# Kernel tuning notes

Measured on AMD Instinct MI355X. Metric: run time of the kernel, lower is better.

## Reference

```python
import jax, jax.numpy as jnp
import numpy as np

EPS = 1e-5  # torch LayerNorm default


def setup_inputs() -> dict:
    key = jax.random.key(0)
    ks = jax.random.split(key, 7)
    B, s, i, c, h = 1, 1024, 512, 8, 8
    scale = 0.1
    return {
        "m": jax.random.normal(ks[0], (B, s, i, c), dtype=jnp.float32),
        "ln_gamma": jnp.ones((c,), dtype=jnp.float32),
        "ln_beta": jnp.zeros((c,), dtype=jnp.float32),
        "Wq": jax.random.normal(ks[1], (c * h, c), dtype=jnp.float32) * scale,
        "Wk": jax.random.normal(ks[2], (c, c), dtype=jnp.float32) * scale,
        "Wv": jax.random.normal(ks[3], (c, c), dtype=jnp.float32) * scale,
        "Wg": jax.random.normal(ks[4], (c * h, c), dtype=jnp.float32) * scale,
        "Wo": jax.random.normal(ks[5], (c, c * h), dtype=jnp.float32) * scale,
        "bo": jnp.zeros((c,), dtype=jnp.float32),
    }


def reference(m, ln_gamma, ln_beta, Wq, Wk, Wv, Wg, Wo, bo):
    c = Wk.shape[0]
    h = Wq.shape[0] // c
    B, s, i, _ = m.shape

    # LayerNorm over the channel dim c
    mu = jnp.mean(m, axis=-1, keepdims=True)
    var = jnp.mean(jnp.square(m - mu), axis=-1, keepdims=True)
    x = (m - mu) * jax.lax.rsqrt(var + EPS) * ln_gamma + ln_beta  # (B,s,i,c)

    # projections (torch Linear: y = x @ W.T)
    q = (x @ Wq.T).reshape(B, s, i, h, c).mean(axis=1)            # (B,i,h,c) mean-pooled query
    k = x @ Wk.T                                                   # (B,s,i,c)
    v = x @ Wv.T                                                   # (B,s,i,c)
    gate = jax.nn.sigmoid(x @ Wg.T).reshape(B, s, i, h, c)        # (B,s,i,h,c)

    # attention logits over the column axis t (=s), softmax along t (dim=-3 of b t i h)
    a = jnp.einsum('bihc,btic->btih', q, k) * (c ** -0.5)          # (B,s,i,h)
    a = jax.nn.softmax(a, axis=1)

    o = gate * jnp.einsum('btih,btic->btihc', a, v)               # (B,s,i,h,c)
    o = o.reshape(B, s, i, h * c)
    return o @ Wo.T + bo                                           # (B,s,i,c)
```

## Files before the change

kernel.cpp:

```cpp
#include <hip/hip_runtime.h>

namespace {
constexpr int S = 1024, I = 512, C = 8, H = 8;
constexpr int R = 4;
constexpr float LNEPS = 1e-5f;
constexpr float SCALE = 0.35355339059327373f;
}

__device__ __forceinline__ float dot8(const float x[8], float4 a, float4 b) {
    float r = x[0] * a.x;
    r += x[1] * a.y; r += x[2] * a.z; r += x[3] * a.w;
    r += x[4] * b.x; r += x[5] * b.y; r += x[6] * b.z; r += x[7] * b.w;
    return r;
}

__device__ __forceinline__ void ln8(float4 a, float4 b, const float gm[8],
                                    const float bt[8], float x[8]) {
    x[0] = a.x; x[1] = a.y; x[2] = a.z; x[3] = a.w;
    x[4] = b.x; x[5] = b.y; x[6] = b.z; x[7] = b.w;
    float mu = 0.f;
#pragma unroll
    for (int c = 0; c < 8; c++) mu += x[c];
    mu *= 0.125f;
    float var = 0.f;
#pragma unroll
    for (int c = 0; c < 8; c++) { float d = x[c] - mu; var += d * d; }
    var *= 0.125f;
    float inv = rsqrtf(var + LNEPS);
#pragma unroll
    for (int c = 0; c < 8; c++) x[c] = (x[c] - mu) * inv * gm[c] + bt[c];
}

__global__ __launch_bounds__(512) void fused(
    const float* __restrict__ m, const float* __restrict__ gamma,
    const float* __restrict__ beta, const float* __restrict__ Wq,
    const float* __restrict__ Wk, const float* __restrict__ Wv,
    const float* __restrict__ Wg, const float* __restrict__ Wo,
    const float* __restrict__ bo, float* __restrict__ out) {
    __shared__ __align__(16) float sWoT[512];
    __shared__ __align__(16) float swred[8 * 16];
    __shared__ __align__(16) float sxbar[16];
    __shared__ __align__(16) float sqk[128];
    __shared__ __align__(16) float srden[16];

    int t = threadIdx.x;
    int w = t >> 6;
    int col = t & 1;
    int si = t >> 1;
    int i = 2 * blockIdx.x + col;

    {
        int j = t & 63, c2 = t >> 6;
        sWoT[j * 8 + c2] = Wo[c2 * 64 + j];
    }

    float gm[8], bt[8];
#pragma unroll
    for (int c = 0; c < 8; c++) { gm[c] = gamma[c]; bt[c] = beta[c]; }

    const float4* m4 = (const float4*)m;
    float x[R][8];
    float acc[8];
#pragma unroll
    for (int c = 0; c < 8; c++) acc[c] = 0.f;
#pragma unroll
    for (int r = 0; r < R; r++) {
        int row = (si + 256 * r) * I + i;
        ln8(m4[row * 2], m4[row * 2 + 1], gm, bt, x[r]);
#pragma unroll
        for (int c = 0; c < 8; c++) acc[c] += x[r][c];
    }
#pragma unroll
    for (int d = 2; d < 64; d <<= 1)
#pragma unroll
        for (int c = 0; c < 8; c++) acc[c] += __shfl_xor(acc[c], d, 64);
    if ((t & 63) < 2) {
#pragma unroll
        for (int c = 0; c < 8; c++) swred[w * 16 + col * 8 + c] = acc[c];
    }
    __syncthreads();
    if (t < 16) {
        float s = 0.f;
#pragma unroll
        for (int ww = 0; ww < 8; ww++) s += swred[ww * 16 + t];
        sxbar[t] = s;
    }
    __syncthreads();
    if (t < 128) {
        int qcol = t >> 6, h = (t >> 3) & 7, c2 = t & 7;
        float xb[8];
#pragma unroll
        for (int c3 = 0; c3 < 8; c3++) xb[c3] = sxbar[qcol * 8 + c3];
        float a = 0.f;
#pragma unroll
        for (int c = 0; c < 8; c++) {
            float qc = 0.f;
#pragma unroll
            for (int c3 = 0; c3 < 8; c3++)
                qc += xb[c3] * Wq[(h * 8 + c) * 8 + c3];
            a += qc * Wk[c * 8 + c2];
        }
        sqk[qcol * 64 + h * 8 + c2] = a * (SCALE / 1024.0f);
    }
    __syncthreads();

    const float4* sqk4 = (const float4*)sqk;
    float p[R][8];
    float e[8];
#pragma unroll
    for (int h = 0; h < 8; h++) {
        float4 q0 = sqk4[col * 16 + h * 2], q1 = sqk4[col * 16 + h * 2 + 1];
        float s = 0.f;
#pragma unroll
        for (int r = 0; r < R; r++) {
            p[r][h] = __expf(dot8(x[r], q0, q1));
            s += p[r][h];
        }
        e[h] = s;
    }
#pragma unroll
    for (int d = 2; d < 64; d <<= 1)
#pragma unroll
        for (int h = 0; h < 8; h++) e[h] += __shfl_xor(e[h], d, 64);
    if ((t & 63) < 2) {
#pragma unroll
        for (int h = 0; h < 8; h++) swred[w * 16 + col * 8 + h] = e[h];
    }
    __syncthreads();
    if (t < 16) {
        float s = 0.f;
#pragma unroll
        for (int ww = 0; ww < 8; ww++) s += swred[ww * 16 + t];
        srden[t] = 1.0f / s;
    }
    __syncthreads();

    const float4* Wv4 = (const float4*)Wv;
    const float4* Wg4 = (const float4*)Wg;
    const float4* sWoT4 = (const float4*)sWoT;

    float v[R][8];
#pragma unroll
    for (int c = 0; c < 8; c++) {
        float4 w0 = Wv4[c * 2], w1 = Wv4[c * 2 + 1];
#pragma unroll
        for (int r = 0; r < R; r++) v[r][c] = dot8(x[r], w0, w1);
    }

    float oacc[R][8];
#pragma unroll
    for (int r = 0; r < R; r++)
#pragma unroll
        for (int c2 = 0; c2 < 8; c2++) oacc[r][c2] = bo[c2];

#pragma unroll 1
    for (int h = 0; h < 8; h++) {
        float rd = srden[col * 8 + h];
        float a_[R];
#pragma unroll
        for (int r = 0; r < R; r++) a_[r] = p[r][h] * rd;
#pragma unroll
        for (int c = 0; c < 8; c++) {
            int hc = h * 8 + c;
            float4 wg0 = Wg4[hc * 2], wg1 = Wg4[hc * 2 + 1];
            float o_[R];
#pragma unroll
            for (int r = 0; r < R; r++) {
                float z = dot8(x[r], wg0, wg1);
                float gate = __builtin_amdgcn_rcpf(1.0f + __expf(-z));
                o_[r] = gate * a_[r] * v[r][c];
            }
            float4 wo0 = sWoT4[hc * 2], wo1 = sWoT4[hc * 2 + 1];
#pragma unroll
            for (int r = 0; r < R; r++) {
                oacc[r][0] += o_[r] * wo0.x; oacc[r][1] += o_[r] * wo0.y;
                oacc[r][2] += o_[r] * wo0.z; oacc[r][3] += o_[r] * wo0.w;
                oacc[r][4] += o_[r] * wo1.x; oacc[r][5] += o_[r] * wo1.y;
                oacc[r][6] += o_[r] * wo1.z; oacc[r][7] += o_[r] * wo1.w;
            }
        }
    }
    float4* out4 = (float4*)out;
#pragma unroll
    for (int r = 0; r < R; r++) {
        int row = (si + 256 * r) * I + i;
        out4[row * 2] = make_float4(oacc[r][0], oacc[r][1], oacc[r][2], oacc[r][3]);
        out4[row * 2 + 1] = make_float4(oacc[r][4], oacc[r][5], oacc[r][6], oacc[r][7]);
    }
}

extern "C" void kernel_launch(void* const* d_in, const int* in_sizes, int n_in,
                              void* d_out, int out_size, void* d_ws, size_t ws_size,
                              hipStream_t stream) {
    const float* m     = (const float*)d_in[0];
    const float* gamma = (const float*)d_in[1];
    const float* beta  = (const float*)d_in[2];
    const float* Wq    = (const float*)d_in[3];
    const float* Wk    = (const float*)d_in[4];
    const float* Wv    = (const float*)d_in[5];
    const float* Wg    = (const float*)d_in[6];
    const float* Wo    = (const float*)d_in[7];
    const float* bo    = (const float*)d_in[8];
    float* out = (float*)d_out;

    fused<<<I / 2, 512, 0, stream>>>(m, gamma, beta, Wq, Wk, Wv, Wg, Wo, bo, out);
}
```

Baseline: 112.3 us.

## Use one column per 256-thread block and compute V per channel inside main loop

Each block now handles a single column i with 256 threads, giving 512 blocks instead of 256 blocks of 512 threads, with launch bounds asking for 3 blocks per CU. V is no longer precomputed into a 4x8 register array but computed per channel inside the loop, and the softmax normalization is folded into p beforehand. The aim is lower register pressure and more resident waves, traded for more full-wave shuffle reductions and redundant per-block loads of Wo and the qk setup.

```diff
diff --git a/kernel.cpp b/kernel.cpp
--- a/kernel.cpp
+++ b/kernel.cpp
@@ -31,26 +31,26 @@
     for (int c = 0; c < 8; c++) x[c] = (x[c] - mu) * inv * gm[c] + bt[c];
 }
 
-__global__ __launch_bounds__(512) void fused(
+__global__ __launch_bounds__(256, 3) void fused(
     const float* __restrict__ m, const float* __restrict__ gamma,
     const float* __restrict__ beta, const float* __restrict__ Wq,
     const float* __restrict__ Wk, const float* __restrict__ Wv,
     const float* __restrict__ Wg, const float* __restrict__ Wo,
     const float* __restrict__ bo, float* __restrict__ out) {
     __shared__ __align__(16) float sWoT[512];
-    __shared__ __align__(16) float swred[8 * 16];
-    __shared__ __align__(16) float sxbar[16];
-    __shared__ __align__(16) float sqk[128];
-    __shared__ __align__(16) float srden[16];
+    __shared__ __align__(16) float swred[4 * 8];
+    __shared__ __align__(16) float sxbar[8];
+    __shared__ __align__(16) float sqk[64];
+    __shared__ __align__(16) float srden[8];
 
     int t = threadIdx.x;
     int w = t >> 6;
-    int col = t & 1;
-    int si = t >> 1;
-    int i = 2 * blockIdx.x + col;
+    int i = blockIdx.x;
 
-    {
-        int j = t & 63, c2 = t >> 6;
+#pragma unroll
+    for (int k = 0; k < 2; k++) {
+        int idx = t + 256 * k;
+        int j = idx & 63, c2 = idx >> 6;
         sWoT[j * 8 + c2] = Wo[c2 * 64 + j];
     }
 
@@ -65,87 +65,78 @@
     for (int c = 0; c < 8; c++) acc[c] = 0.f;
 #pragma unroll
     for (int r = 0; r < R; r++) {
-        int row = (si + 256 * r) * I + i;
+        int row = (t + 256 * r) * I + i;
         ln8(m4[row * 2], m4[row * 2 + 1], gm, bt, x[r]);
 #pragma unroll
         for (int c = 0; c < 8; c++) acc[c] += x[r][c];
     }
 #pragma unroll
-    for (int d = 2; d < 64; d <<= 1)
+    for (int d = 1; d < 64; d <<= 1)
 #pragma unroll
         for (int c = 0; c < 8; c++) acc[c] += __shfl_xor(acc[c], d, 64);
-    if ((t & 63) < 2) {
+    if ((t & 63) == 0) {
 #pragma unroll
-        for (int c = 0; c < 8; c++) swred[w * 16 + col * 8 + c] = acc[c];
+        for (int c = 0; c < 8; c++) swred[w * 8 + c] = acc[c];
     }
     __syncthreads();
-    if (t < 16) {
-        float s = 0.f;
-#pragma unroll
-        for (int ww = 0; ww < 8; ww++) s += swred[ww * 16 + t];
-        sxbar[t] = s;
-    }
+    if (t < 8)
+        sxbar[t] = swred[t] + swred[8 + t] + swred[16 + t] + swred[24 + t];
     __syncthreads();
-    if (t < 128) {
-        int qcol = t >> 6, h = (t >> 3) & 7, c2 = t & 7;
-        float xb[8];
-#pragma unroll
-        for (int c3 = 0; c3 < 8; c3++) xb[c3] = sxbar[qcol * 8 + c3];
+    if (t < 64) {
+        int h = t >> 3, c2 = t & 7;
         float a = 0.f;
 #pragma unroll
         for (int c = 0; c < 8; c++) {
             float qc = 0.f;
 #pragma unroll
             for (int c3 = 0; c3 < 8; c3++)
-                qc += xb[c3] * Wq[(h * 8 + c) * 8 + c3];
+                qc += sxbar[c3] * Wq[(h * 8 + c) * 8 + c3];
             a += qc * Wk[c * 8 + c2];
         }
-        sqk[qcol * 64 + h * 8 + c2] = a * (SCALE / 1024.0f);
+        sqk[t] = a * (SCALE / 1024.0f);
     }
     __syncthreads();
 
     const float4* sqk4 = (const float4*)sqk;
     float p[R][8];
-    float e[8];
+    {
+        float e[8];
+#pragma unroll
+        for (int h = 0; h < 8; h++) {
+            float4 q0 = sqk4[h * 2], q1 = sqk4[h * 2 + 1];
+            float s = 0.f;
+#pragma unroll
+            for (int r = 0; r < R; r++) {
+                p[r][h] = __expf(dot8(x[r], q0, q1));
+                s += p[r][h];
+            }
+            e[h] = s;
+        }
+#pragma unroll
+        for (int d = 1; d < 64; d <<= 1)
+#pragma unroll
+            for (int h = 0; h < 8; h++) e[h] += __shfl_xor(e[h], d, 64);
+        if ((t & 63) == 0) {
+#pragma unroll
+            for (int h = 0; h < 8; h++) swred[w * 8 + h] = e[h];
+        }
+    }
+    __syncthreads();
+    if (t < 8)
+        srden[t] =
+            1.0f / (swred[t] + swred[8 + t] + swred[16 + t] + swred[24 + t]);
+    __syncthreads();
+
 #pragma unroll
     for (int h = 0; h < 8; h++) {
-        float4 q0 = sqk4[col * 16 + h * 2], q1 = sqk4[col * 16 + h * 2 + 1];
-        float s = 0.f;
+        float rd = srden[h];
 #pragma unroll
-        for (int r = 0; r < R; r++) {
-            p[r][h] = __expf(dot8(x[r], q0, q1));
-            s += p[r][h];
-        }
-        e[h] = s;
+        for (int r = 0; r < R; r++) p[r][h] *= rd;
     }
-#pragma unroll
-    for (int d = 2; d < 64; d <<= 1)
-#pragma unroll
-        for (int h = 0; h < 8; h++) e[h] += __shfl_xor(e[h], d, 64);
-    if ((t & 63) < 2) {
-#pragma unroll
-        for (int h = 0; h < 8; h++) swred[w * 16 + col * 8 + h] = e[h];
-    }
-    __syncthreads();
-    if (t < 16) {
-        float s = 0.f;
-#pragma unroll
-        for (int ww = 0; ww < 8; ww++) s += swred[ww * 16 + t];
-        srden[t] = 1.0f / s;
-    }
-    __syncthreads();
 
     const float4* Wv4 = (const float4*)Wv;
     const float4* Wg4 = (const float4*)Wg;
     const float4* sWoT4 = (const float4*)sWoT;
-
-    float v[R][8];
-#pragma unroll
-    for (int c = 0; c < 8; c++) {
-        float4 w0 = Wv4[c * 2], w1 = Wv4[c * 2 + 1];
-#pragma unroll
-        for (int r = 0; r < R; r++) v[r][c] = dot8(x[r], w0, w1);
-    }
 
     float oacc[R][8];
 #pragma unroll
@@ -154,23 +145,23 @@
         for (int c2 = 0; c2 < 8; c2++) oacc[r][c2] = bo[c2];
 
 #pragma unroll 1
-    for (int h = 0; h < 8; h++) {
-        float rd = srden[col * 8 + h];
-        float a_[R];
+    for (int c = 0; c < 8; c++) {
+        float4 wv0 = Wv4[c * 2], wv1 = Wv4[c * 2 + 1];
+        float vr[R];
 #pragma unroll
-        for (int r = 0; r < R; r++) a_[r] = p[r][h] * rd;
-#pragma unroll
-        for (int c = 0; c < 8; c++) {
+        for (int r = 0; r < R; r++) vr[r] = dot8(x[r], wv0, wv1);
+#pragma unroll 2
+        for (int h = 0; h < 8; h++) {
             int hc = h * 8 + c;
             float4 wg0 = Wg4[hc * 2], wg1 = Wg4[hc * 2 + 1];
+            float4 wo0 = sWoT4[hc * 2], wo1 = sWoT4[hc * 2 + 1];
             float o_[R];
 #pragma unroll
             for (int r = 0; r < R; r++) {
                 float z = dot8(x[r], wg0, wg1);
                 float gate = __builtin_amdgcn_rcpf(1.0f + __expf(-z));
-                o_[r] = gate * a_[r] * v[r][c];
+                o_[r] = gate * p[r][h] * vr[r];
             }
-            float4 wo0 = sWoT4[hc * 2], wo1 = sWoT4[hc * 2 + 1];
 #pragma unroll
             for (int r = 0; r < R; r++) {
                 oacc[r][0] += o_[r] * wo0.x; oacc[r][1] += o_[r] * wo0.y;
@@ -183,7 +174,7 @@
     float4* out4 = (float4*)out;
 #pragma unroll
     for (int r = 0; r < R; r++) {
-        int row = (si + 256 * r) * I + i;
+        int row = (t + 256 * r) * I + i;
         out4[row * 2] = make_float4(oacc[r][0], oacc[r][1], oacc[r][2], oacc[r][3]);
         out4[row * 2 + 1] = make_float4(oacc[r][4], oacc[r][5], oacc[r][6], oacc[r][7]);
     }
@@ -203,5 +194,5 @@
     const float* bo    = (const float*)d_in[8];
     float* out = (float*)d_out;
 
-    fused<<<I / 2, 512, 0, stream>>>(m, gamma, beta, Wq, Wk, Wv, Wg, Wo, bo, out);
+    fused<<<I, 256, 0, stream>>>(m, gamma, beta, Wq, Wk, Wv, Wg, Wo, bo, out);
 }
```

Measured after the change: 123.7 us. 1.1x slower.
